# Kernel optimization log

Measured on AMD Instinct MI355X. Metric: run time of the kernel, lower is better.

The kernel has to match this reference:

```python
import jax, jax.numpy as jnp
import numpy as np
from jax import lax

UNITS = 2048
INPUT_DIM = 128
T = 4096
SR = 0.9
LR = 0.1
CONNECTIVITY = 0.1
INPUT_SCALING = 1.0


def setup_inputs() -> dict:
    key = jax.random.key(0)
    k1, k2, k3, k4 = jax.random.split(key, 4)
    Win = (jax.random.uniform(k1, (UNITS, INPUT_DIM), dtype=jnp.float32) * 2.0 - 1.0) * INPUT_SCALING
    # W: sparse normal, keep entries with prob = connectivity
    W = jax.random.normal(k2, (UNITS, UNITS), dtype=jnp.float32)
    keep = jax.random.uniform(k3, (UNITS, UNITS)) <= CONNECTIVITY
    W = jnp.where(keep, W, 0.0)
    # scale to target spectral radius (init-time, matches torch eigvals scaling)
    rho = float(np.max(np.abs(np.linalg.eigvals(np.asarray(W)))))
    W = W * (SR / rho)
    input_sequence = jax.random.normal(k4, (T, INPUT_DIM), dtype=jnp.float32)
    initial_state = jnp.zeros((1, UNITS), dtype=jnp.float32)
    return {
        "input_sequence": input_sequence,
        "initial_state": initial_state,
        "W": W,
        "Win": Win,
    }


def reference(input_sequence, initial_state, W, Win):
    # Leaky-tanh ESN recurrence:
    def step(state, u):  # state: [1, units], u: [input_dim]
        pre = state @ W.T + u @ Win.T          # [1, units]
        new_state = (1.0 - LR) * state + LR * jnp.tanh(pre)
        return new_state, new_state[0]

    final_state, history = lax.scan(step, initial_state, input_sequence)
    return history, final_state
```

## Files before the change

### kernel.cpp

```cpp
#include <hip/hip_runtime.h>

#define UNITS   2048
#define IN_DIM  128
#define T_STEPS 4096
#define NBLK    64
#define TPB     512
#define BROWS   32

typedef unsigned int u32;
typedef u32 u32x4 __attribute__((ext_vector_type(4)));
typedef u32 u32x2v __attribute__((ext_vector_type(2)));
typedef short short8 __attribute__((ext_vector_type(8)));
typedef __bf16 bf16x8 __attribute__((ext_vector_type(8)));
typedef float f32x4 __attribute__((ext_vector_type(4)));

__global__ void esn_init(u32* __restrict__ buf) {
    int i = blockIdx.x * blockDim.x + threadIdx.x;
    if (i < 2 * UNITS) buf[i] = 0u;
}

__device__ __forceinline__ unsigned short f2bf(float f) {
    u32 x = __float_as_uint(f);
    return (unsigned short)((x + 0x7FFFu + ((x >> 16) & 1u)) >> 16);
}

__global__ void __launch_bounds__(TPB, 2) esn_step(
    const float* __restrict__ inp,
    const float* __restrict__ s0,
    const float* __restrict__ W,
    const float* __restrict__ Win,
    float* __restrict__ out,
    u32* __restrict__ buf)
{
    const int b    = blockIdx.x;
    const int tid  = threadIdx.x;
    const int lane = tid & 63;
    const int wv   = tid >> 3 >> 3;
    const int h8   = (lane >> 4) * 8;
    const int colr = lane & 15;

    __shared__ unsigned short sB[UNITS];
    __shared__ float red[2][8][2][16];
    __shared__ float s_state[BROWS];
    __shared__ u32 cnt_mm[2];

    const int rbase = b * BROWS;
    bf16x8 a0[8], a1[8];
    #pragma unroll
    for (int tt = 0; tt < 8; ++tt) {
        const int kb = wv * 256 + tt * 32 + h8;
        short8 t0, t1;
        #pragma unroll
        for (int j = 0; j < 8; ++j) {
            t0[j] = (short)f2bf(W[(size_t)(rbase + colr) * UNITS + kb + j]);
            t1[j] = (short)f2bf(W[(size_t)(rbase + 16 + colr) * UNITS + kb + j]);
        }
        a0[tt] = *(bf16x8*)&t0;
        a1[tt] = *(bf16x8*)&t1;
    }
    bf16x8 ain0 = {}, ain1 = {};
    const bool hasIn = (wv < 4);
    if (hasIn) {
        const int kb = wv * 32 + h8;
        short8 t0, t1;
        #pragma unroll
        for (int j = 0; j < 8; ++j) {
            t0[j] = (short)f2bf(Win[(size_t)(rbase + colr) * IN_DIM + kb + j]);
            t1[j] = (short)f2bf(Win[(size_t)(rbase + 16 + colr) * IN_DIM + kb + j]);
        }
        ain0 = *(bf16x8*)&t0;
        ain1 = *(bf16x8*)&t1;
    }

    {
        float4 v = *(const float4*)(s0 + tid * 4);
        u32x2v pk;
        pk[0] = (u32)f2bf(v.x) | ((u32)f2bf(v.y) << 16);
        pk[1] = (u32)f2bf(v.z) | ((u32)f2bf(v.w) << 16);
        *(u32x2v*)&sB[tid * 4] = pk;
    }
    if (tid < BROWS) s_state[tid] = s0[rbase + tid];
    if (tid == 0) { cnt_mm[0] = 0u; cnt_mm[1] = 0u; }
    __syncthreads();

    for (int t = 0; t < T_STEPS; ++t) {
        const int par   = t & 1;
        const u32 epoch = (u32)(t >> 1) + 1u;
        const u32 tag   = (u32)t;

        const u32* pp = buf + par * UNITS + tid * 4;
        u32x4 A;
        if (t > 0)
            asm volatile("global_load_dwordx4 %0, %1, off sc0 sc1"
                         : "=v"(A) : "v"(pp) : "memory");

        float4 iA, iB;
        if (hasIn) {
            const float* ip = inp + (size_t)t * IN_DIM + wv * 32 + h8;
            iA = *(const float4*)ip;
            iB = *(const float4*)(ip + 4);
        }

        if (t > 0) {
            while (true) {
                asm volatile("s_waitcnt vmcnt(0)" : "+v"(A) :: "memory");
                bool ok = ((A[0] >> 16) == tag) & ((A[1] >> 16) == tag)
                        & ((A[2] >> 16) == tag) & ((A[3] >> 16) == tag);
                if (ok) break;
                asm volatile("global_load_dwordx4 %0, %1, off sc0 sc1"
                             : "=v"(A) : "v"(pp) : "memory");
            }
            u32x2v pk;
            pk[0] = (A[0] & 0xFFFFu) | (A[1] << 16);
            pk[1] = (A[2] & 0xFFFFu) | (A[3] << 16);
            *(u32x2v*)&sB[tid * 4] = pk;
        }

        f32x4 c0a = {0.f,0.f,0.f,0.f}, c0b = {0.f,0.f,0.f,0.f};
        f32x4 c1a = {0.f,0.f,0.f,0.f}, c1b = {0.f,0.f,0.f,0.f};
        if (hasIn) {
            short8 si;
            si[0] = (short)f2bf(iA.x); si[1] = (short)f2bf(iA.y);
            si[2] = (short)f2bf(iA.z); si[3] = (short)f2bf(iA.w);
            si[4] = (short)f2bf(iB.x); si[5] = (short)f2bf(iB.y);
            si[6] = (short)f2bf(iB.z); si[7] = (short)f2bf(iB.w);
            bf16x8 bin = *(bf16x8*)&si;
            c0b = __builtin_amdgcn_mfma_f32_16x16x32_bf16(ain0, bin, c0b, 0, 0, 0);
            c1b = __builtin_amdgcn_mfma_f32_16x16x32_bf16(ain1, bin, c1b, 0, 0, 0);
        }
        #pragma unroll
        for (int tt = 0; tt < 8; ++tt) {
            bf16x8 bb = *(const bf16x8*)&sB[wv * 256 + tt * 32 + h8];
            if (tt & 1) {
                c0b = __builtin_amdgcn_mfma_f32_16x16x32_bf16(a0[tt], bb, c0b, 0, 0, 0);
                c1b = __builtin_amdgcn_mfma_f32_16x16x32_bf16(a1[tt], bb, c1b, 0, 0, 0);
            } else {
                c0a = __builtin_amdgcn_mfma_f32_16x16x32_bf16(a0[tt], bb, c0a, 0, 0, 0);
                c1a = __builtin_amdgcn_mfma_f32_16x16x32_bf16(a1[tt], bb, c1a, 0, 0, 0);
            }
        }
        f32x4 acc0 = c0a + c0b, acc1 = c1a + c1b;

        if (colr == 0) {
            *(f32x4*)&red[par][wv][0][(lane >> 4) * 4] = acc0;
            *(f32x4*)&red[par][wv][1][(lane >> 4) * 4] = acc1;
        }
        u32 rtn = 0;
        if (lane == 0)
            rtn = __hip_atomic_fetch_add(&cnt_mm[par], 1u, __ATOMIC_ACQ_REL,
                                         __HIP_MEMORY_SCOPE_WORKGROUP);
        rtn = __shfl(rtn, 0);

        if (rtn == 8u * epoch - 1u && lane < BROWS) {
            const int rt = lane >> 4, rr = lane & 15;
            float pre = 0.f;
            #pragma unroll
            for (int w8 = 0; w8 < 8; ++w8) pre += red[par][w8][rt][rr];
            float e  = __expf(2.0f * pre);
            float th = 1.0f - 2.0f / (e + 1.0f);
            float sn = 0.9f * s_state[lane] + 0.1f * th;
            s_state[lane] = sn;
            const int j = rbase + lane;
            if (t < T_STEPS - 1) {
                u32 word = ((u32)(t + 1) << 16) | (u32)f2bf(sn);
                u32* ps = buf + ((t + 1) & 1) * UNITS + j;
                asm volatile("global_store_dword %0, %1, off sc0 sc1"
                             :: "v"(ps), "v"(word) : "memory");
            }
            out[(size_t)t * UNITS + j] = sn;
            if (t == T_STEPS - 1) out[(size_t)T_STEPS * UNITS + j] = sn;
        }
    }
}

extern "C" void kernel_launch(void* const* d_in, const int* in_sizes, int n_in,
                              void* d_out, int out_size, void* d_ws, size_t ws_size,
                              hipStream_t stream) {
    const float* inp = (const float*)d_in[0];
    const float* s0  = (const float*)d_in[1];
    const float* W   = (const float*)d_in[2];
    const float* Win = (const float*)d_in[3];
    float* out = (float*)d_out;
    u32* buf = (u32*)d_ws;

    esn_init<<<dim3(16), dim3(256), 0, stream>>>(buf);

    void* args[6];
    args[0] = (void*)&inp; args[1] = (void*)&s0;  args[2] = (void*)&W;
    args[3] = (void*)&Win; args[4] = (void*)&out; args[5] = (void*)&buf;
    hipLaunchCooperativeKernel((void*)esn_step, dim3(NBLK), dim3(TPB), args, 0, stream);
}
```

Baseline: 5.947 ms.

## Halve block count to 32 with 1024 threads and 64 rows per block

Repartitions the persistent cooperative kernel so that 32 blocks of 16 waves each own 64 state rows, instead of 64 blocks of 8 waves owning 32 rows. Each wave now covers a 128-wide K slice across four 16-row tiles, and every wave also handles part of the input projection. The aim is to halve the number of blocks that write and poll the global handoff buffer each step, cutting cross-block synchronisation cost. In exchange, each block does a longer 16-way reduction, runs a heavier last-arriver epilogue, and has less spare parallelism across CUs.

```diff
diff --git a/kernel.cpp b/kernel.cpp
--- a/kernel.cpp
+++ b/kernel.cpp
@@ -3,12 +3,12 @@
 #define UNITS   2048
 #define IN_DIM  128
 #define T_STEPS 4096
-#define NBLK    64
-#define TPB     512
-#define BROWS   32
+#define NBLK    32
+#define TPB     1024
+#define BROWS   64
+#define NWAVE   16
 
 typedef unsigned int u32;
-typedef u32 u32x4 __attribute__((ext_vector_type(4)));
 typedef u32 u32x2v __attribute__((ext_vector_type(2)));
 typedef short short8 __attribute__((ext_vector_type(8)));
 typedef __bf16 bf16x8 __attribute__((ext_vector_type(8)));
@@ -24,7 +24,7 @@
     return (unsigned short)((x + 0x7FFFu + ((x >> 16) & 1u)) >> 16);
 }
 
-__global__ void __launch_bounds__(TPB, 2) esn_step(
+__global__ void __launch_bounds__(TPB, 4) esn_step(
     const float* __restrict__ inp,
     const float* __restrict__ s0,
     const float* __restrict__ W,
@@ -35,49 +35,44 @@
     const int b    = blockIdx.x;
     const int tid  = threadIdx.x;
     const int lane = tid & 63;
-    const int wv   = tid >> 3 >> 3;
+    const int wv   = tid >> 6;
     const int h8   = (lane >> 4) * 8;
     const int colr = lane & 15;
 
     __shared__ unsigned short sB[UNITS];
-    __shared__ float red[2][8][2][16];
+    __shared__ float red[2][NWAVE][4][16];
     __shared__ float s_state[BROWS];
     __shared__ u32 cnt_mm[2];
 
     const int rbase = b * BROWS;
-    bf16x8 a0[8], a1[8];
+    bf16x8 afr[4][4];
     #pragma unroll
-    for (int tt = 0; tt < 8; ++tt) {
-        const int kb = wv * 256 + tt * 32 + h8;
-        short8 t0, t1;
+    for (int rt = 0; rt < 4; ++rt) {
+        const size_t row = (size_t)(rbase + rt * 16 + colr);
         #pragma unroll
-        for (int j = 0; j < 8; ++j) {
-            t0[j] = (short)f2bf(W[(size_t)(rbase + colr) * UNITS + kb + j]);
-            t1[j] = (short)f2bf(W[(size_t)(rbase + 16 + colr) * UNITS + kb + j]);
+        for (int tt = 0; tt < 4; ++tt) {
+            const int kb = wv * 128 + tt * 32 + h8;
+            short8 s;
+            #pragma unroll
+            for (int j = 0; j < 8; ++j) s[j] = (short)f2bf(W[row * UNITS + kb + j]);
+            afr[rt][tt] = *(bf16x8*)&s;
         }
-        a0[tt] = *(bf16x8*)&t0;
-        a1[tt] = *(bf16x8*)&t1;
     }
-    bf16x8 ain0 = {}, ain1 = {};
-    const bool hasIn = (wv < 4);
-    if (hasIn) {
-        const int kb = wv * 32 + h8;
-        short8 t0, t1;
+    const int rt_in = wv & 3, kt_in = wv >> 2;
+    bf16x8 ainf;
+    {
+        const size_t row = (size_t)(rbase + rt_in * 16 + colr);
+        const int kb = kt_in * 32 + h8;
+        short8 s;
         #pragma unroll
-        for (int j = 0; j < 8; ++j) {
-            t0[j] = (short)f2bf(Win[(size_t)(rbase + colr) * IN_DIM + kb + j]);
-            t1[j] = (short)f2bf(Win[(size_t)(rbase + 16 + colr) * IN_DIM + kb + j]);
-        }
-        ain0 = *(bf16x8*)&t0;
-        ain1 = *(bf16x8*)&t1;
+        for (int j = 0; j < 8; ++j) s[j] = (short)f2bf(Win[row * IN_DIM + kb + j]);
+        ainf = *(bf16x8*)&s;
     }
 
     {
-        float4 v = *(const float4*)(s0 + tid * 4);
-        u32x2v pk;
-        pk[0] = (u32)f2bf(v.x) | ((u32)f2bf(v.y) << 16);
-        pk[1] = (u32)f2bf(v.z) | ((u32)f2bf(v.w) << 16);
-        *(u32x2v*)&sB[tid * 4] = pk;
+        float2 v = *(const float2*)(s0 + tid * 2);
+        sB[tid * 2]     = f2bf(v.x);
+        sB[tid * 2 + 1] = f2bf(v.y);
     }
     if (tid < BROWS) s_state[tid] = s0[rbase + tid];
     if (tid == 0) { cnt_mm[0] = 0u; cnt_mm[1] = 0u; }
@@ -88,62 +83,52 @@
         const u32 epoch = (u32)(t >> 1) + 1u;
         const u32 tag   = (u32)t;
 
-        const u32* pp = buf + par * UNITS + tid * 4;
-        u32x4 A;
+        const u32* pp = buf + par * UNITS + tid * 2;
+        u32x2v A;
         if (t > 0)
-            asm volatile("global_load_dwordx4 %0, %1, off sc0 sc1"
+            asm volatile("global_load_dwordx2 %0, %1, off sc0 sc1"
                          : "=v"(A) : "v"(pp) : "memory");
 
-        float4 iA, iB;
-        if (hasIn) {
-            const float* ip = inp + (size_t)t * IN_DIM + wv * 32 + h8;
-            iA = *(const float4*)ip;
-            iB = *(const float4*)(ip + 4);
-        }
+        const float* ip = inp + (size_t)t * IN_DIM + kt_in * 32 + h8;
+        float4 iA = *(const float4*)ip;
+        float4 iB = *(const float4*)(ip + 4);
 
         if (t > 0) {
             while (true) {
                 asm volatile("s_waitcnt vmcnt(0)" : "+v"(A) :: "memory");
-                bool ok = ((A[0] >> 16) == tag) & ((A[1] >> 16) == tag)
-                        & ((A[2] >> 16) == tag) & ((A[3] >> 16) == tag);
+                bool ok = ((A[0] >> 16) == tag) & ((A[1] >> 16) == tag);
                 if (ok) break;
-                asm volatile("global_load_dwordx4 %0, %1, off sc0 sc1"
+                asm volatile("global_load_dwordx2 %0, %1, off sc0 sc1"
                              : "=v"(A) : "v"(pp) : "memory");
             }
-            u32x2v pk;
-            pk[0] = (A[0] & 0xFFFFu) | (A[1] << 16);
-            pk[1] = (A[2] & 0xFFFFu) | (A[3] << 16);
-            *(u32x2v*)&sB[tid * 4] = pk;
+            u32 pk = (A[0] & 0xFFFFu) | (A[1] << 16);
+            *(u32*)&sB[tid * 2] = pk;
         }
 
-        f32x4 c0a = {0.f,0.f,0.f,0.f}, c0b = {0.f,0.f,0.f,0.f};
-        f32x4 c1a = {0.f,0.f,0.f,0.f}, c1b = {0.f,0.f,0.f,0.f};
-        if (hasIn) {
+        f32x4 acc[4];
+        {
             short8 si;
             si[0] = (short)f2bf(iA.x); si[1] = (short)f2bf(iA.y);
             si[2] = (short)f2bf(iA.z); si[3] = (short)f2bf(iA.w);
             si[4] = (short)f2bf(iB.x); si[5] = (short)f2bf(iB.y);
             si[6] = (short)f2bf(iB.z); si[7] = (short)f2bf(iB.w);
             bf16x8 bin = *(bf16x8*)&si;
-            c0b = __builtin_amdgcn_mfma_f32_16x16x32_bf16(ain0, bin, c0b, 0, 0, 0);
-            c1b = __builtin_amdgcn_mfma_f32_16x16x32_bf16(ain1, bin, c1b, 0, 0, 0);
+            f32x4 z = {0.f, 0.f, 0.f, 0.f};
+            acc[0] = z; acc[1] = z; acc[2] = z; acc[3] = z;
+            acc[rt_in] = __builtin_amdgcn_mfma_f32_16x16x32_bf16(ainf, bin, acc[rt_in], 0, 0, 0);
         }
         #pragma unroll
-        for (int tt = 0; tt < 8; ++tt) {
-            bf16x8 bb = *(const bf16x8*)&sB[wv * 256 + tt * 32 + h8];
-            if (tt & 1) {
-                c0b = __builtin_amdgcn_mfma_f32_16x16x32_bf16(a0[tt], bb, c0b, 0, 0, 0);
-                c1b = __builtin_amdgcn_mfma_f32_16x16x32_bf16(a1[tt], bb, c1b, 0, 0, 0);
-            } else {
-                c0a = __builtin_amdgcn_mfma_f32_16x16x32_bf16(a0[tt], bb, c0a, 0, 0, 0);
-                c1a = __builtin_amdgcn_mfma_f32_16x16x32_bf16(a1[tt], bb, c1a, 0, 0, 0);
-            }
+        for (int tt = 0; tt < 4; ++tt) {
+            bf16x8 bb = *(const bf16x8*)&sB[wv * 128 + tt * 32 + h8];
+            #pragma unroll
+            for (int rt = 0; rt < 4; ++rt)
+                acc[rt] = __builtin_amdgcn_mfma_f32_16x16x32_bf16(afr[rt][tt], bb, acc[rt], 0, 0, 0);
         }
-        f32x4 acc0 = c0a + c0b, acc1 = c1a + c1b;
 
         if (colr == 0) {
-            *(f32x4*)&red[par][wv][0][(lane >> 4) * 4] = acc0;
-            *(f32x4*)&red[par][wv][1][(lane >> 4) * 4] = acc1;
+            #pragma unroll
+            for (int rt = 0; rt < 4; ++rt)
+                *(f32x4*)&red[par][wv][rt][(lane >> 4) * 4] = acc[rt];
         }
         u32 rtn = 0;
         if (lane == 0)
@@ -151,11 +136,11 @@
                                          __HIP_MEMORY_SCOPE_WORKGROUP);
         rtn = __shfl(rtn, 0);
 
-        if (rtn == 8u * epoch - 1u && lane < BROWS) {
+        if (rtn == (u32)NWAVE * epoch - 1u) {
             const int rt = lane >> 4, rr = lane & 15;
             float pre = 0.f;
             #pragma unroll
-            for (int w8 = 0; w8 < 8; ++w8) pre += red[par][w8][rt][rr];
+            for (int w = 0; w < NWAVE; ++w) pre += red[par][w][rt][rr];
             float e  = __expf(2.0f * pre);
             float th = 1.0f - 2.0f / (e + 1.0f);
             float sn = 0.9f * s_state[lane] + 0.1f * th;
```

Result: slower. 10.53 ms (+77.1%).
